# Kernel optimization log

Measured on AMD Instinct MI355X. Metric: run time of the kernel, lower is better.

## Reference

```python
import jax, jax.numpy as jnp
import numpy as np

B = 128
H = 512
S_TOK = 512
S_DESC = 128
N_NODES = 65536
MARGIN = 0.05
COS_EPS = 1e-8


def setup_inputs() -> dict:
    key = jax.random.key(0)
    ks = jax.random.split(key, 26)
    sc = 1.0 / np.sqrt(H)
    inp = {
        "token_feat": jax.random.normal(ks[0], (B, S_TOK, H), jnp.float32),
        "token_len": jnp.maximum(jax.random.randint(ks[1], (B,), 0, S_TOK), 1),
        "node_h": jax.random.normal(ks[2], (N_NODES, H), jnp.float32),
        "seg_ids": jnp.sort(jax.random.randint(ks[3], (N_NODES,), 0, B)),
        "desc_anchor_feat": jax.random.normal(ks[4], (B, S_DESC, H), jnp.float32),
        "desc_anchor_len": jnp.maximum(jax.random.randint(ks[5], (B,), 0, S_DESC), 1),
        "desc_neg_feat": jax.random.normal(ks[6], (B, S_DESC, H), jnp.float32),
        "desc_neg_len": jnp.maximum(jax.random.randint(ks[7], (B,), 0, S_DESC), 1),
        # attention params: Linear(H,H) weight/bias, Linear(H,1) weight/bias
        "Wt": jax.random.normal(ks[8], (H, H), jnp.float32) * sc,
        "bt": jax.random.normal(ks[9], (H,), jnp.float32) * sc,
        "vt": jax.random.normal(ks[10], (H,), jnp.float32) * sc,
        "ct": jax.random.normal(ks[11], (), jnp.float32) * sc,
        "Wa": jax.random.normal(ks[12], (H, H), jnp.float32) * sc,
        "ba": jax.random.normal(ks[13], (H,), jnp.float32) * sc,
        "va": jax.random.normal(ks[14], (H,), jnp.float32) * sc,
        "ca": jax.random.normal(ks[15], (), jnp.float32) * sc,
        "Wd": jax.random.normal(ks[16], (H, H), jnp.float32) * sc,
        "bd": jax.random.normal(ks[17], (H,), jnp.float32) * sc,
        "vd": jax.random.normal(ks[18], (H,), jnp.float32) * sc,
        "cd": jax.random.normal(ks[19], (), jnp.float32) * sc,
        "Wf": jax.random.normal(ks[20], (2 * H, H), jnp.float32) * sc,
        "bf": jax.random.normal(ks[21], (H,), jnp.float32) * sc,
    }
    return inp


def masked_attn_pool(feat, lens, W, b, v, c):
    # feat: [B,S,H]; lens: [B]. Masked softmax attention pooling == the
    # per-sample masked_select + softmax + bmm loop, vectorized.
    logits = jnp.einsum("bsh,h->bs", jnp.tanh(jnp.einsum("bsh,hk->bsk", feat, W) + b), v) + c
    mask = jnp.arange(feat.shape[1])[None, :] < lens[:, None]
    logits = jnp.where(mask, logits, -jnp.inf)
    w = jax.nn.softmax(logits, axis=1)  # [B,S]
    return jnp.einsum("bs,bsh->bh", w, feat)


def segment_attn_pool(h, seg, W, b, v, c, num_segments):
    # h: [N,H] packed node states; seg: [N] sample id. Per-segment softmax attn
    # pooling == the per-sample slice + softmax + bmm loop over tree_node_num.
    logits = jnp.tanh(h @ W + b) @ v + c  # [N]
    m = jax.ops.segment_max(logits, seg, num_segments=num_segments)
    e = jnp.exp(logits - m[seg])
    denom = jax.ops.segment_sum(e, seg, num_segments=num_segments)
    w = e / denom[seg]
    return jax.ops.segment_sum(w[:, None] * h, seg, num_segments=num_segments)


def cosine_sim(a, b):
    na = jnp.maximum(jnp.linalg.norm(a, axis=1), COS_EPS)
    nb = jnp.maximum(jnp.linalg.norm(b, axis=1), COS_EPS)
    return jnp.sum(a * b, axis=1) / (na * nb)


def reference(token_feat, token_len, node_h, seg_ids, desc_anchor_feat,
              desc_anchor_len, desc_neg_feat, desc_neg_len,
              Wt, bt, vt, ct, Wa, ba, va, ca, Wd, bd, vd, cd, Wf, bf):
    # token modality (use_token_attn, then use_tanh)
    tok = jnp.tanh(masked_attn_pool(token_feat, token_len, Wt, bt, vt, ct))
    # AST modality: use_tanh applies to node states BEFORE attention
    hn = jnp.tanh(node_h)
    ast = jnp.tanh(segment_attn_pool(hn, seg_ids, Wa, ba, va, ca, B))
    code_feat = jnp.tanh(jnp.concatenate([tok, ast], axis=1) @ Wf + bf)
    # desc modality: attn pool, use_tanh, then the extra unconditional tanh
    da = jnp.tanh(jnp.tanh(masked_attn_pool(desc_anchor_feat, desc_anchor_len, Wd, bd, vd, cd)))
    dn = jnp.tanh(jnp.tanh(masked_attn_pool(desc_neg_feat, desc_neg_len, Wd, bd, vd, cd)))
    anchor_sim = cosine_sim(code_feat, da)
    neg_sim = cosine_sim(code_feat, dn)
    loss = jnp.mean(jnp.maximum(MARGIN - anchor_sim + neg_sim, 1e-6))
    return loss
```

## Files before the change

kernel.cpp:

```cpp
#include <hip/hip_runtime.h>
#include <math.h>

#define HDIM 512
#define BATCH 128

typedef _Float16 f16x8 __attribute__((ext_vector_type(8)));
typedef float f32x4 __attribute__((ext_vector_type(4)));

__device__ __forceinline__ float fast_tanh(float x) {
  float e = __expf(2.0f * x);
  return 1.0f - 2.0f / (e + 1.0f);
}

__device__ __forceinline__ void gload_lds16(const void* g, void* l) {
  __builtin_amdgcn_global_load_lds(
      (const __attribute__((address_space(1))) unsigned int*)g,
      (__attribute__((address_space(3))) unsigned int*)l, 16, 0, 0);
}


__global__ __launch_bounds__(256) void cvt_frag_kernel(
    const float* __restrict__ tok, const float* __restrict__ node,
    const float* __restrict__ da, const float* __restrict__ dn,
    _Float16* __restrict__ A2tok, _Float16* __restrict__ A2node,
    _Float16* __restrict__ A2desc) {
  const int seg = blockIdx.y;
  const float* A;
  _Float16* A2;
  int M16, rb_base, rb_bits;
  bool do_tanh = false;
  if (seg == 0)      { A = tok;  A2 = A2tok;  M16 = 4096; rb_base = 0;    rb_bits = 12; }
  else if (seg == 1) { A = node; A2 = A2node; M16 = 4096; rb_base = 0;    rb_bits = 12; do_tanh = true; }
  else if (seg == 2) { A = da;   A2 = A2desc; M16 = 2048; rb_base = 0;    rb_bits = 10; }
  else               { A = dn;   A2 = A2desc; M16 = 2048; rb_base = 1024; rb_bits = 10; }
  const int lane = threadIdx.x & 63, wid = threadIdx.x >> 6;
  const int total = 16 << rb_bits;
  const int rl = lane & 15, kc = lane >> 4;
  for (int fl = blockIdx.x * 4 + wid; fl < total; fl += gridDim.x * 4) {
    const int frag = fl >> rb_bits;
    const int rb_local = fl & ((1 << rb_bits) - 1);
    const int rb = rb_base + rb_local;
    const int kt = frag >> 1, ks = frag & 1;
    const int row_src = rb_local * 16 + rl;
    const int k = kt * 64 + ks * 32 + kc * 8;
    const float4* src = (const float4*)(A + (size_t)row_src * HDIM + k);
    const float4 x = src[0];
    const float4 y = src[1];
    f16x8 h;
    if (do_tanh) {
      h[0] = (_Float16)fast_tanh(x.x); h[1] = (_Float16)fast_tanh(x.y);
      h[2] = (_Float16)fast_tanh(x.z); h[3] = (_Float16)fast_tanh(x.w);
      h[4] = (_Float16)fast_tanh(y.x); h[5] = (_Float16)fast_tanh(y.y);
      h[6] = (_Float16)fast_tanh(y.z); h[7] = (_Float16)fast_tanh(y.w);
    } else {
      h[0] = (_Float16)x.x; h[1] = (_Float16)x.y;
      h[2] = (_Float16)x.z; h[3] = (_Float16)x.w;
      h[4] = (_Float16)y.x; h[5] = (_Float16)y.y;
      h[6] = (_Float16)y.z; h[7] = (_Float16)y.w;
    }
    *(f16x8*)(A2 + ((size_t)frag * M16 + rb) * 512 + lane * 8) = h;
  }
}

__global__ __launch_bounds__(256) void cvt_w3_kernel(
    const float* __restrict__ Wt, const float* __restrict__ Wa,
    const float* __restrict__ Wd, _Float16* __restrict__ W2t,
    _Float16* __restrict__ W2a, _Float16* __restrict__ W2d) {
  const int i = blockIdx.x * 256 + threadIdx.x;
  if (i >= 512 * 64) return;
  const float* W = (blockIdx.y == 0) ? Wt : (blockIdx.y == 1) ? Wa : Wd;
  _Float16* W2 = (blockIdx.y == 0) ? W2t : (blockIdx.y == 1) ? W2a : W2d;
  const int n = i & 511, g = i >> 9;
  const int kt = g >> 3, cc = g & 7;
  f16x8 h;
#pragma unroll
  for (int j = 0; j < 8; ++j)
    h[j] = (_Float16)W[(size_t)(kt * 64 + cc * 8 + j) * HDIM + n];
  char* dst = (char*)W2 + ((size_t)kt * 512 + n) * 128 + ((cc * 16) ^ ((n & 7) << 4));
  *(f16x8*)dst = h;
}

__global__ __launch_bounds__(256, 2) void gemm_logits_frag_kernel(
    const _Float16* __restrict__ A2tok, const _Float16* __restrict__ A2node,
    const _Float16* __restrict__ A2desc,
    const _Float16* __restrict__ W2t, const _Float16* __restrict__ W2a,
    const _Float16* __restrict__ W2d,
    const float* __restrict__ bt, const float* __restrict__ vt,
    const float* __restrict__ ba, const float* __restrict__ va,
    const float* __restrict__ bd, const float* __restrict__ vd,
    float* __restrict__ logits_tok, float* __restrict__ logits_node,
    float* __restrict__ logits_desc) {
  __shared__ __align__(16) _Float16 Bs[2][256 * 64];

  const int tid = threadIdx.x;
  const int raw = (int)blockIdx.x;
  const int swz = (raw & 7) * 320 + (raw >> 3);

  int id, local;
  if (swz < 1024)      { id = 0; local = swz; }
  else if (swz < 2048) { id = 1; local = swz - 1024; }
  else                 { id = 2; local = swz - 2048; }
  const int mb = local >> 1, nb = local & 1;
  const _Float16* A2 = (id == 0) ? A2tok : (id == 1) ? A2node : A2desc;
  const _Float16* W2 = (id == 0) ? W2t : (id == 1) ? W2a : W2d;
  const float* bias = (id == 0) ? bt : (id == 1) ? ba : bd;
  const float* vvec = (id == 0) ? vt : (id == 1) ? va : vd;
  float* logits = (id == 0) ? logits_tok : (id == 1) ? logits_node : logits_desc;
  const int M16 = (id == 2) ? 2048 : 4096;
  const size_t m0 = (size_t)mb * 128;
  const int n0 = nb * 256;

  const int lane = tid & 63, wid = tid >> 6;
  const int tx = lane & 15, qd = lane >> 4;
  const int wm = wid >> 1;
  const int wn = wid & 1;

  const _Float16* aBase = A2 + ((size_t)(m0 >> 4) + wm * 4) * 512 + lane * 8;
  const char* gB = (const char*)W2 + (size_t)n0 * 128;

  f32x4 acc[4][8];
#pragma unroll
  for (int i = 0; i < 4; ++i)
#pragma unroll
    for (int j = 0; j < 8; ++j) acc[i][j] = (f32x4){0.f, 0.f, 0.f, 0.f};

  f16x8 aR[2][2][4];

  auto LOAD_A = [&](int par, int kt) {
#pragma unroll
    for (int ks = 0; ks < 2; ++ks)
#pragma unroll
      for (int i = 0; i < 4; ++i)
        aR[par][ks][i] =
            *(const f16x8*)(aBase + ((size_t)(kt * 2 + ks) * M16 + i) * 512);
  };
  auto STAGE_B = [&](int buf, int kt) {
    const char* b = gB + (size_t)kt * 65536;
#pragma unroll
    for (int p = 0; p < 8; ++p)
      gload_lds16(b + tid * 16 + p * 4096, (char*)Bs[buf] + tid * 16 + p * 4096);
  };
  auto COMPUTE = [&](int par, int buf) {
#pragma unroll
    for (int ks = 0; ks < 2; ++ks) {
#pragma unroll
      for (int half = 0; half < 2; ++half) {
        f16x8 bF[4];
#pragma unroll
        for (int f = 0; f < 4; ++f) {
          const int n = wn * 128 + (half * 4 + f) * 16 + tx;
          int by = n * 128 + ((ks * 64 + qd * 16) ^ ((n & 7) << 4));
          bF[f] = *(const f16x8*)((const char*)Bs[buf] + by);
        }
        __builtin_amdgcn_s_setprio(1);
#pragma unroll
        for (int i = 0; i < 4; ++i)
#pragma unroll
          for (int f = 0; f < 4; ++f)
            acc[i][half * 4 + f] = __builtin_amdgcn_mfma_f32_16x16x32_f16(
                aR[par][ks][i], bF[f], acc[i][half * 4 + f], 0, 0, 0);
        __builtin_amdgcn_s_setprio(0);
      }
    }
  };

  LOAD_A(0, 0);
  STAGE_B(0, 0);
#pragma unroll
  for (int t = 0; t < 8; ++t) {
    const int cur = t & 1;
    if (t < 7) {
      LOAD_A(cur ^ 1, t + 1);
      STAGE_B(cur ^ 1, t + 1);
      asm volatile("s_waitcnt vmcnt(16)" ::: "memory");
    } else {
      asm volatile("s_waitcnt vmcnt(0)" ::: "memory");
    }
    __builtin_amdgcn_s_barrier();
    asm volatile("" ::: "memory");
    COMPUTE(cur, cur);
    asm volatile("" ::: "memory");
    __builtin_amdgcn_s_barrier();
    asm volatile("" ::: "memory");
  }

  float vv[8], bb[8];
#pragma unroll
  for (int j = 0; j < 8; ++j) {
    const int n = n0 + wn * 128 + j * 16 + tx;
    vv[j] = vvec[n];
    bb[j] = bias[n];
  }
#pragma unroll
  for (int i = 0; i < 4; ++i) {
#pragma unroll
    for (int r = 0; r < 4; ++r) {
      float s = 0.0f;
#pragma unroll
      for (int j = 0; j < 8; ++j)
        s = fmaf(vv[j], fast_tanh(acc[i][j][r] + bb[j]), s);
      s += __shfl_xor(s, 1);
      s += __shfl_xor(s, 2);
      s += __shfl_xor(s, 4);
      s += __shfl_xor(s, 8);
      if (tx == 0)
        atomicAdd(&logits[m0 + wm * 64 + i * 16 + qd * 4 + r], s);
    }
  }
}


__global__ void zero_kernel(float* __restrict__ p, int n) {
  const int i = blockIdx.x * 256 + threadIdx.x;
  if (i < n) p[i] = 0.0f;
}

__global__ void seg_bounds_kernel(const int* __restrict__ seg, int N,
                                  int* __restrict__ seg_start) {
  const int b = threadIdx.x;
  if (b > BATCH) return;
  int lo = 0, hi = N;
  while (lo < hi) {
    const int mid = (lo + hi) >> 1;
    if (seg[mid] < b) lo = mid + 1; else hi = mid;
  }
  seg_start[b] = lo;
}

__global__ __launch_bounds__(256) void softmax_all_kernel(
    float* __restrict__ ltok, float* __restrict__ ldesc,
    float* __restrict__ lnode, const int* __restrict__ tlen,
    const int* __restrict__ dalen, const int* __restrict__ dnlen,
    const int* __restrict__ seg_start) {
  __shared__ float smax[4], ssum[4];
  const int b = blockIdx.x, mode = blockIdx.y, tid = threadIdx.x;
  float* l;
  int s0, s1, fill_end;
  if (mode == 0)      { l = ltok + (size_t)b * 512;          s0 = 0; s1 = tlen[b];  fill_end = 512; }
  else if (mode == 1) { l = ldesc + (size_t)b * 128;         s0 = 0; s1 = dalen[b]; fill_end = 128; }
  else if (mode == 2) { l = ldesc + 16384 + (size_t)b * 128; s0 = 0; s1 = dnlen[b]; fill_end = 128; }
  else                { l = lnode; s0 = seg_start[b]; s1 = seg_start[b + 1]; fill_end = -1; }

  float mymax = -1e30f;
  for (int s = s0 + tid; s < s1; s += 256) mymax = fmaxf(mymax, l[s]);
#pragma unroll
  for (int off = 32; off; off >>= 1) mymax = fmaxf(mymax, __shfl_xor(mymax, off));
  if ((tid & 63) == 0) smax[tid >> 6] = mymax;
  __syncthreads();
  const float bmax = fmaxf(fmaxf(smax[0], smax[1]), fmaxf(smax[2], smax[3]));
  float mysum = 0.0f;
  for (int s = s0 + tid; s < s1; s += 256) mysum += __expf(l[s] - bmax);
#pragma unroll
  for (int off = 32; off; off >>= 1) mysum += __shfl_xor(mysum, off);
  if ((tid & 63) == 0) ssum[tid >> 6] = mysum;
  __syncthreads();
  const float inv = 1.0f / (ssum[0] + ssum[1] + ssum[2] + ssum[3]);
  for (int s = s0 + tid; s < s1; s += 256) l[s] = __expf(l[s] - bmax) * inv;
  if (fill_end > 0)
    for (int s = s1 + tid; s < fill_end; s += 256) l[s] = 0.0f;
}

__device__ __forceinline__ unsigned frag_read2(
    const _Float16* __restrict__ A2, int M16, int row, int h) {
  const int frag = (h >> 6) * 2 + ((h >> 5) & 1);
  const int lane = (row & 15) + (((h >> 3) & 3) << 4);
  const size_t off = ((size_t)frag * M16 + (row >> 4)) * 512 + lane * 8 + (h & 7);
  return *(const unsigned*)((const char*)A2 + off * 2);
}

__global__ __launch_bounds__(256) void pool_masked_all_kernel(
    const _Float16* __restrict__ A2tok, const _Float16* __restrict__ A2desc,
    const float* __restrict__ ltok, const float* __restrict__ ldesc,
    float* __restrict__ tok_pool, float* __restrict__ da_pool,
    float* __restrict__ dn_pool) {
  const int b = blockIdx.x, c = blockIdx.y, tid = threadIdx.x;
  const _Float16* A2;
  const float* w;
  float* out;
  int M16, rbase, s0;
  if (c < 8)       { A2 = A2tok;  M16 = 4096; rbase = b * 512;         w = ltok;  out = tok_pool; s0 = c * 64; }
  else if (c < 10) { A2 = A2desc; M16 = 2048; rbase = b * 128;         w = ldesc; out = da_pool;  s0 = (c - 8) * 64; }
  else             { A2 = A2desc; M16 = 2048; rbase = 16384 + b * 128; w = ldesc; out = dn_pool;  s0 = (c - 10) * 64; }
  const int h = tid * 2;
  float ax = 0.0f, ay = 0.0f;
  for (int s = s0; s < s0 + 64; ++s) {
    const int row = rbase + s;
    const float wsc = w[row];
    if (wsc != 0.0f) {
      const unsigned u = frag_read2(A2, M16, row, h);
      const _Float16* hp = (const _Float16*)&u;
      ax = fmaf(wsc, (float)hp[0], ax);
      ay = fmaf(wsc, (float)hp[1], ay);
    }
  }
  atomicAdd(&out[b * HDIM + h], ax);
  atomicAdd(&out[b * HDIM + h + 1], ay);
}

__global__ __launch_bounds__(256) void pool_tiled_seg_kernel(
    const _Float16* __restrict__ A2, const float* __restrict__ w,
    const int* __restrict__ seg_start, float* __restrict__ pool) {
  const int b = blockIdx.x, c = blockIdx.y, tid = threadIdx.x;
  const int h = tid * 2;
  const int s0 = seg_start[b], s1 = seg_start[b + 1];
  const int nseg = s1 - s0;
  const int chunk = (nseg + (int)gridDim.y - 1) / (int)gridDim.y;
  const int a0 = s0 + c * chunk;
  const int a1 = min(s1, a0 + chunk);
  float ax = 0.0f, ay = 0.0f;
  for (int s = a0; s < a1; ++s) {
    const float wsc = w[s];
    const unsigned u = frag_read2(A2, 4096, s, h);
    const _Float16* hp = (const _Float16*)&u;
    ax = fmaf(wsc, (float)hp[0], ax);
    ay = fmaf(wsc, (float)hp[1], ay);
  }
  atomicAdd(&pool[b * HDIM + h], ax);
  atomicAdd(&pool[b * HDIM + h + 1], ay);
}

__global__ __launch_bounds__(256) void code_gemm_kernel(
    const float* __restrict__ tok_pool, const float* __restrict__ ast_pool,
    const float* __restrict__ Wf, float* __restrict__ parts) {
  __shared__ float catS[128][65];
  __shared__ float4 wfS[64][32];
  const int nb = blockIdx.x, kb = blockIdx.y, tid = threadIdx.x;
  const int k0 = kb * 64;
  const float* src = (k0 < 512) ? (tok_pool + k0) : (ast_pool + (k0 - 512));
  for (int i = tid; i < 128 * 16; i += 256) {
    const int r = i >> 4, c4 = i & 15;
    const float4 v = *(const float4*)(src + (size_t)r * HDIM + c4 * 4);
    catS[r][c4 * 4 + 0] = fast_tanh(v.x);
    catS[r][c4 * 4 + 1] = fast_tanh(v.y);
    catS[r][c4 * 4 + 2] = fast_tanh(v.z);
    catS[r][c4 * 4 + 3] = fast_tanh(v.w);
  }
  for (int i = tid; i < 64 * 32; i += 256) {
    const int r = i >> 5, c = i & 31;
    wfS[r][c] = *(const float4*)(Wf + (size_t)(k0 + r) * HDIM + nb * 128 + c * 4);
  }
  __syncthreads();
  const int tb = tid >> 4, tn = tid & 15;
  const int b0 = tb * 8, n0l = tn * 8;
  float acc[8][8];
#pragma unroll
  for (int i = 0; i < 8; ++i)
#pragma unroll
    for (int j = 0; j < 8; ++j) acc[i][j] = 0.0f;
  for (int k = 0; k < 64; ++k) {
    float a[8];
#pragma unroll
    for (int i = 0; i < 8; ++i) a[i] = catS[b0 + i][k];
    const float4 w0 = wfS[k][tn * 2], w1 = wfS[k][tn * 2 + 1];
    const float wv[8] = {w0.x, w0.y, w0.z, w0.w, w1.x, w1.y, w1.z, w1.w};
#pragma unroll
    for (int i = 0; i < 8; ++i)
#pragma unroll
      for (int j = 0; j < 8; ++j) acc[i][j] = fmaf(a[i], wv[j], acc[i][j]);
  }
  float* dst = parts + ((size_t)kb * 128) * HDIM + nb * 128;
#pragma unroll
  for (int i = 0; i < 8; ++i) {
    const float4 o0 = {acc[i][0], acc[i][1], acc[i][2], acc[i][3]};
    const float4 o1 = {acc[i][4], acc[i][5], acc[i][6], acc[i][7]};
    *(float4*)(dst + (size_t)(b0 + i) * HDIM + n0l) = o0;
    *(float4*)(dst + (size_t)(b0 + i) * HDIM + n0l + 4) = o1;
  }
}

__global__ __launch_bounds__(256) void sims_kernel(
    const float* __restrict__ parts, const float* __restrict__ bfv,
    const float* __restrict__ da_pool, const float* __restrict__ dn_pool,
    float* __restrict__ terms) {
  __shared__ float sr[4][5];
  const int b = blockIdx.x, tid = threadIdx.x;
  float c2 = 0, a2 = 0, n2 = 0, ca = 0, cn = 0;
  for (int i = tid; i < HDIM; i += 256) {
    float pre = bfv[i];
#pragma unroll
    for (int kb = 0; kb < 16; ++kb)
      pre += parts[((size_t)kb * 128 + b) * HDIM + i];
    const float cf = fast_tanh(pre);
    const float av = fast_tanh(fast_tanh(da_pool[(size_t)b * HDIM + i]));
    const float nv = fast_tanh(fast_tanh(dn_pool[(size_t)b * HDIM + i]));
    c2 = fmaf(cf, cf, c2); a2 = fmaf(av, av, a2); n2 = fmaf(nv, nv, n2);
    ca = fmaf(cf, av, ca); cn = fmaf(cf, nv, cn);
  }
#pragma unroll
  for (int off = 32; off; off >>= 1) {
    c2 += __shfl_xor(c2, off); a2 += __shfl_xor(a2, off); n2 += __shfl_xor(n2, off);
    ca += __shfl_xor(ca, off); cn += __shfl_xor(cn, off);
  }
  const int wv = tid >> 6;
  if ((tid & 63) == 0) {
    sr[wv][0] = c2; sr[wv][1] = a2; sr[wv][2] = n2; sr[wv][3] = ca; sr[wv][4] = cn;
  }
  __syncthreads();
  if (tid == 0) {
    c2 = sr[0][0] + sr[1][0] + sr[2][0] + sr[3][0];
    a2 = sr[0][1] + sr[1][1] + sr[2][1] + sr[3][1];
    n2 = sr[0][2] + sr[1][2] + sr[2][2] + sr[3][2];
    ca = sr[0][3] + sr[1][3] + sr[2][3] + sr[3][3];
    cn = sr[0][4] + sr[1][4] + sr[2][4] + sr[3][4];
    const float nc = fmaxf(sqrtf(c2), 1e-8f);
    const float na = fmaxf(sqrtf(a2), 1e-8f);
    const float nn = fmaxf(sqrtf(n2), 1e-8f);
    terms[b] = fmaxf(0.05f - ca / (nc * na) + cn / (nc * nn), 1e-6f);
  }
}

__global__ void loss_kernel(const float* __restrict__ terms, float* __restrict__ out) {
  const int tid = threadIdx.x;
  float v = terms[tid];
#pragma unroll
  for (int off = 32; off; off >>= 1) v += __shfl_xor(v, off);
  __shared__ float sr[2];
  if ((tid & 63) == 0) sr[tid >> 6] = v;
  __syncthreads();
  if (tid == 0) out[0] = (sr[0] + sr[1]) * (1.0f / (float)BATCH);
}


extern "C" void kernel_launch(void* const* d_in, const int* in_sizes, int n_in,
                              void* d_out, int out_size, void* d_ws, size_t ws_size,
                              hipStream_t stream) {
  (void)in_sizes; (void)n_in; (void)out_size; (void)ws_size;
  const float* token_feat = (const float*)d_in[0];
  const int*   token_len  = (const int*)d_in[1];
  const float* node_h     = (const float*)d_in[2];
  const int*   seg_ids    = (const int*)d_in[3];
  const float* da_feat    = (const float*)d_in[4];
  const int*   da_len     = (const int*)d_in[5];
  const float* dn_feat    = (const float*)d_in[6];
  const int*   dn_len     = (const int*)d_in[7];
  const float* Wt = (const float*)d_in[8];
  const float* bt = (const float*)d_in[9];
  const float* vt = (const float*)d_in[10];
  const float* Wa = (const float*)d_in[12];
  const float* ba = (const float*)d_in[13];
  const float* va = (const float*)d_in[14];
  const float* Wd = (const float*)d_in[16];
  const float* bd = (const float*)d_in[17];
  const float* vd = (const float*)d_in[18];
  const float* Wf  = (const float*)d_in[20];
  const float* bfv = (const float*)d_in[21];

  const int MTOK = 65536;
  const int MDESC2 = 32768;
  const int NNODES = 65536;

  float* ws = (float*)d_ws;
  float* logits_tok  = ws;
  float* logits_node = logits_tok + MTOK;
  float* logits_desc = logits_node + NNODES;
  float* tok_pool    = logits_desc + MDESC2;
  float* ast_pool    = tok_pool + 128 * HDIM;
  float* da_pool     = ast_pool + 128 * HDIM;
  float* dn_pool     = da_pool + 128 * HDIM;
  float* terms       = dn_pool + 128 * HDIM;
  int*   seg_start   = (int*)(terms + 128);
  float* parts       = (float*)(seg_start + 256);
  _Float16* W2t = (_Float16*)(parts + 16 * 128 * HDIM);
  _Float16* W2a = W2t + HDIM * HDIM;
  _Float16* W2d = W2a + HDIM * HDIM;
  _Float16* A2tok  = W2d + HDIM * HDIM;
  _Float16* A2node = A2tok + (size_t)MTOK * 512;
  _Float16* A2desc = A2node + (size_t)NNODES * 512;

  const int ZTOT = MTOK + NNODES + MDESC2 + 4 * 128 * HDIM;
  zero_kernel<<<dim3((ZTOT + 255) / 256), 256, 0, stream>>>(ws, ZTOT);
  seg_bounds_kernel<<<1, 256, 0, stream>>>(seg_ids, NNODES, seg_start);

  cvt_w3_kernel<<<dim3(128, 3), 256, 0, stream>>>(Wt, Wa, Wd, W2t, W2a, W2d);
  cvt_frag_kernel<<<dim3(4096, 4), 256, 0, stream>>>(
      token_feat, node_h, da_feat, dn_feat, A2tok, A2node, A2desc);

  gemm_logits_frag_kernel<<<2560, 256, 0, stream>>>(
      A2tok, A2node, A2desc, W2t, W2a, W2d,
      bt, vt, ba, va, bd, vd, logits_tok, logits_node, logits_desc);

  softmax_all_kernel<<<dim3(BATCH, 4), 256, 0, stream>>>(
      logits_tok, logits_desc, logits_node, token_len, da_len, dn_len, seg_start);

  pool_masked_all_kernel<<<dim3(BATCH, 12), 256, 0, stream>>>(
      A2tok, A2desc, logits_tok, logits_desc, tok_pool, da_pool, dn_pool);
  pool_tiled_seg_kernel<<<dim3(BATCH, 4), 256, 0, stream>>>(
      A2node, logits_node, seg_start, ast_pool);

  code_gemm_kernel<<<dim3(4, 16), 256, 0, stream>>>(tok_pool, ast_pool, Wf, parts);
  sims_kernel<<<BATCH, 256, 0, stream>>>(parts, bfv, da_pool, dn_pool, terms);
  loss_kernel<<<1, 128, 0, stream>>>(terms, (float*)d_out);
}
```

Baseline: 309.6 us.

## Fuse fp32-to-fp16 conversion into token/desc GEMM and pool from fp32 inputs

The token and description inputs are no longer converted into a separate fp16 fragment buffer. A new GEMM kernel loads fp32 A rows directly, converts them in registers and feeds the MFMAs, with staggered waitcnt pipelining across the two k-substeps. The masked pooling kernel now reads the original fp32 features instead of the fp16 fragments. Only the node path keeps the tanh+convert prepass. This removes a large write and re-read of intermediate fp16 data, but the GEMM reads twice as many A bytes and uses less efficient A access patterns.

```diff
diff --git a/kernel.cpp b/kernel.cpp
--- a/kernel.cpp
+++ b/kernel.cpp
@@ -19,46 +19,25 @@
 }
 
 
-__global__ __launch_bounds__(256) void cvt_frag_kernel(
-    const float* __restrict__ tok, const float* __restrict__ node,
-    const float* __restrict__ da, const float* __restrict__ dn,
-    _Float16* __restrict__ A2tok, _Float16* __restrict__ A2node,
-    _Float16* __restrict__ A2desc) {
-  const int seg = blockIdx.y;
-  const float* A;
-  _Float16* A2;
-  int M16, rb_base, rb_bits;
-  bool do_tanh = false;
-  if (seg == 0)      { A = tok;  A2 = A2tok;  M16 = 4096; rb_base = 0;    rb_bits = 12; }
-  else if (seg == 1) { A = node; A2 = A2node; M16 = 4096; rb_base = 0;    rb_bits = 12; do_tanh = true; }
-  else if (seg == 2) { A = da;   A2 = A2desc; M16 = 2048; rb_base = 0;    rb_bits = 10; }
-  else               { A = dn;   A2 = A2desc; M16 = 2048; rb_base = 1024; rb_bits = 10; }
+__global__ __launch_bounds__(256) void cvt_frag_node_kernel(
+    const float* __restrict__ node, _Float16* __restrict__ A2node) {
   const int lane = threadIdx.x & 63, wid = threadIdx.x >> 6;
-  const int total = 16 << rb_bits;
   const int rl = lane & 15, kc = lane >> 4;
-  for (int fl = blockIdx.x * 4 + wid; fl < total; fl += gridDim.x * 4) {
-    const int frag = fl >> rb_bits;
-    const int rb_local = fl & ((1 << rb_bits) - 1);
-    const int rb = rb_base + rb_local;
+  for (int fl = blockIdx.x * 4 + wid; fl < 65536; fl += gridDim.x * 4) {
+    const int frag = fl >> 12;
+    const int rb = fl & 4095;
     const int kt = frag >> 1, ks = frag & 1;
-    const int row_src = rb_local * 16 + rl;
+    const int row = rb * 16 + rl;
     const int k = kt * 64 + ks * 32 + kc * 8;
-    const float4* src = (const float4*)(A + (size_t)row_src * HDIM + k);
+    const float4* src = (const float4*)(node + (size_t)row * HDIM + k);
     const float4 x = src[0];
     const float4 y = src[1];
     f16x8 h;
-    if (do_tanh) {
-      h[0] = (_Float16)fast_tanh(x.x); h[1] = (_Float16)fast_tanh(x.y);
-      h[2] = (_Float16)fast_tanh(x.z); h[3] = (_Float16)fast_tanh(x.w);
-      h[4] = (_Float16)fast_tanh(y.x); h[5] = (_Float16)fast_tanh(y.y);
-      h[6] = (_Float16)fast_tanh(y.z); h[7] = (_Float16)fast_tanh(y.w);
-    } else {
-      h[0] = (_Float16)x.x; h[1] = (_Float16)x.y;
-      h[2] = (_Float16)x.z; h[3] = (_Float16)x.w;
-      h[4] = (_Float16)y.x; h[5] = (_Float16)y.y;
-      h[6] = (_Float16)y.z; h[7] = (_Float16)y.w;
-    }
-    *(f16x8*)(A2 + ((size_t)frag * M16 + rb) * 512 + lane * 8) = h;
+    h[0] = (_Float16)fast_tanh(x.x); h[1] = (_Float16)fast_tanh(x.y);
+    h[2] = (_Float16)fast_tanh(x.z); h[3] = (_Float16)fast_tanh(x.w);
+    h[4] = (_Float16)fast_tanh(y.x); h[5] = (_Float16)fast_tanh(y.y);
+    h[6] = (_Float16)fast_tanh(y.z); h[7] = (_Float16)fast_tanh(y.w);
+    *(f16x8*)(A2node + ((size_t)frag * 4096 + rb) * 512 + lane * 8) = h;
   }
 }
 
@@ -80,40 +59,22 @@
   *(f16x8*)dst = h;
 }
 
-__global__ __launch_bounds__(256, 2) void gemm_logits_frag_kernel(
-    const _Float16* __restrict__ A2tok, const _Float16* __restrict__ A2node,
-    const _Float16* __restrict__ A2desc,
-    const _Float16* __restrict__ W2t, const _Float16* __restrict__ W2a,
-    const _Float16* __restrict__ W2d,
-    const float* __restrict__ bt, const float* __restrict__ vt,
-    const float* __restrict__ ba, const float* __restrict__ va,
-    const float* __restrict__ bd, const float* __restrict__ vd,
-    float* __restrict__ logits_tok, float* __restrict__ logits_node,
-    float* __restrict__ logits_desc) {
+__global__ __launch_bounds__(256, 2) void gemm_logits_node_kernel(
+    const _Float16* __restrict__ A2, const _Float16* __restrict__ W2,
+    const float* __restrict__ bias, const float* __restrict__ vvec,
+    float* __restrict__ logits) {
   __shared__ __align__(16) _Float16 Bs[2][256 * 64];
 
   const int tid = threadIdx.x;
   const int raw = (int)blockIdx.x;
-  const int swz = (raw & 7) * 320 + (raw >> 3);
-
-  int id, local;
-  if (swz < 1024)      { id = 0; local = swz; }
-  else if (swz < 2048) { id = 1; local = swz - 1024; }
-  else                 { id = 2; local = swz - 2048; }
-  const int mb = local >> 1, nb = local & 1;
-  const _Float16* A2 = (id == 0) ? A2tok : (id == 1) ? A2node : A2desc;
-  const _Float16* W2 = (id == 0) ? W2t : (id == 1) ? W2a : W2d;
-  const float* bias = (id == 0) ? bt : (id == 1) ? ba : bd;
-  const float* vvec = (id == 0) ? vt : (id == 1) ? va : vd;
-  float* logits = (id == 0) ? logits_tok : (id == 1) ? logits_node : logits_desc;
-  const int M16 = (id == 2) ? 2048 : 4096;
+  const int swz = (raw & 7) * 128 + (raw >> 3);
+  const int mb = swz >> 1, nb = swz & 1;
   const size_t m0 = (size_t)mb * 128;
   const int n0 = nb * 256;
 
   const int lane = tid & 63, wid = tid >> 6;
   const int tx = lane & 15, qd = lane >> 4;
-  const int wm = wid >> 1;
-  const int wn = wid & 1;
+  const int wm = wid >> 1, wn = wid & 1;
 
   const _Float16* aBase = A2 + ((size_t)(m0 >> 4) + wm * 4) * 512 + lane * 8;
   const char* gB = (const char*)W2 + (size_t)n0 * 128;
@@ -132,7 +93,7 @@
 #pragma unroll
       for (int i = 0; i < 4; ++i)
         aR[par][ks][i] =
-            *(const f16x8*)(aBase + ((size_t)(kt * 2 + ks) * M16 + i) * 512);
+            *(const f16x8*)(aBase + ((size_t)(kt * 2 + ks) * 4096 + i) * 512);
   };
   auto STAGE_B = [&](int buf, int kt) {
     const char* b = gB + (size_t)kt * 65536;
@@ -179,6 +140,170 @@
     __builtin_amdgcn_s_barrier();
     asm volatile("" ::: "memory");
     COMPUTE(cur, cur);
+    asm volatile("" ::: "memory");
+    __builtin_amdgcn_s_barrier();
+    asm volatile("" ::: "memory");
+  }
+
+  float vv[8], bb[8];
+#pragma unroll
+  for (int j = 0; j < 8; ++j) {
+    const int n = n0 + wn * 128 + j * 16 + tx;
+    vv[j] = vvec[n];
+    bb[j] = bias[n];
+  }
+#pragma unroll
+  for (int i = 0; i < 4; ++i) {
+#pragma unroll
+    for (int r = 0; r < 4; ++r) {
+      float s = 0.0f;
+#pragma unroll
+      for (int j = 0; j < 8; ++j)
+        s = fmaf(vv[j], fast_tanh(acc[i][j][r] + bb[j]), s);
+      s += __shfl_xor(s, 1);
+      s += __shfl_xor(s, 2);
+      s += __shfl_xor(s, 4);
+      s += __shfl_xor(s, 8);
+      if (tx == 0)
+        atomicAdd(&logits[m0 + wm * 64 + i * 16 + qd * 4 + r], s);
+    }
+  }
+}
+
+__global__ __launch_bounds__(256, 2) void gemm_logits_f32a_kernel(
+    const float* __restrict__ A_tok, const float* __restrict__ A_da,
+    const float* __restrict__ A_dn,
+    const _Float16* __restrict__ W2t, const _Float16* __restrict__ W2d,
+    const float* __restrict__ bt, const float* __restrict__ vt,
+    const float* __restrict__ bd, const float* __restrict__ vd,
+    float* __restrict__ logits_tok, float* __restrict__ logits_desc) {
+  __shared__ __align__(16) _Float16 Bs[2][256 * 64];
+
+  const int tid = threadIdx.x;
+  const int raw = (int)blockIdx.x;
+  const int swz = (raw & 7) * 192 + (raw >> 3);
+
+  int id, local;
+  if (swz < 1024) { id = 0; local = swz; }
+  else            { id = 1; local = swz - 1024; }
+  const int mb = local >> 1, nb = local & 1;
+  const size_t m0 = (size_t)mb * 128;
+  const int n0 = nb * 256;
+  const float* A;
+  size_t m_src;
+  if (id == 0)            { A = A_tok; m_src = m0; }
+  else if (m0 < 16384)    { A = A_da;  m_src = m0; }
+  else                    { A = A_dn;  m_src = m0 - 16384; }
+  const _Float16* W2 = id ? W2d : W2t;
+  const float* bias = id ? bd : bt;
+  const float* vvec = id ? vd : vt;
+  float* logits = id ? logits_desc : logits_tok;
+
+  const int lane = tid & 63, wid = tid >> 6;
+  const int tx = lane & 15, qd = lane >> 4;
+  const int wm = wid >> 1, wn = wid & 1;
+
+  const float* aB32 = A + (m_src + wm * 64 + (lane & 15)) * (size_t)HDIM + (lane >> 4) * 8;
+  const char* gB = (const char*)W2 + (size_t)n0 * 128;
+
+  f32x4 acc[4][8];
+#pragma unroll
+  for (int i = 0; i < 4; ++i)
+#pragma unroll
+    for (int j = 0; j < 8; ++j) acc[i][j] = (f32x4){0.f, 0.f, 0.f, 0.f};
+
+  float4 f0[4][2], f1[4][2];
+  f16x8 aR[4];
+
+  auto STAGE_B = [&](int buf, int kt) {
+    const char* b = gB + (size_t)kt * 65536;
+#pragma unroll
+    for (int p = 0; p < 8; ++p)
+      gload_lds16(b + tid * 16 + p * 4096, (char*)Bs[buf] + tid * 16 + p * 4096);
+  };
+  auto LOADA0 = [&](int kt) {
+#pragma unroll
+    for (int i = 0; i < 4; ++i) {
+      const float* p = aB32 + (size_t)i * 8192 + kt * 64;
+      f0[i][0] = ((const float4*)p)[0];
+      f0[i][1] = ((const float4*)p)[1];
+    }
+  };
+  auto LOADA1 = [&](int kt) {
+#pragma unroll
+    for (int i = 0; i < 4; ++i) {
+      const float* p = aB32 + (size_t)i * 8192 + kt * 64 + 32;
+      f1[i][0] = ((const float4*)p)[0];
+      f1[i][1] = ((const float4*)p)[1];
+    }
+  };
+  auto CVT0 = [&]() {
+#pragma unroll
+    for (int i = 0; i < 4; ++i) {
+      f16x8 h;
+      h[0] = (_Float16)f0[i][0].x; h[1] = (_Float16)f0[i][0].y;
+      h[2] = (_Float16)f0[i][0].z; h[3] = (_Float16)f0[i][0].w;
+      h[4] = (_Float16)f0[i][1].x; h[5] = (_Float16)f0[i][1].y;
+      h[6] = (_Float16)f0[i][1].z; h[7] = (_Float16)f0[i][1].w;
+      aR[i] = h;
+    }
+  };
+  auto CVT1 = [&]() {
+#pragma unroll
+    for (int i = 0; i < 4; ++i) {
+      f16x8 h;
+      h[0] = (_Float16)f1[i][0].x; h[1] = (_Float16)f1[i][0].y;
+      h[2] = (_Float16)f1[i][0].z; h[3] = (_Float16)f1[i][0].w;
+      h[4] = (_Float16)f1[i][1].x; h[5] = (_Float16)f1[i][1].y;
+      h[6] = (_Float16)f1[i][1].z; h[7] = (_Float16)f1[i][1].w;
+      aR[i] = h;
+    }
+  };
+  auto MFMA_KS = [&](int buf, int ks) {
+#pragma unroll
+    for (int half = 0; half < 2; ++half) {
+      f16x8 bF[4];
+#pragma unroll
+      for (int f = 0; f < 4; ++f) {
+        const int n = wn * 128 + (half * 4 + f) * 16 + tx;
+        int by = n * 128 + ((ks * 64 + qd * 16) ^ ((n & 7) << 4));
+        bF[f] = *(const f16x8*)((const char*)Bs[buf] + by);
+      }
+      __builtin_amdgcn_s_setprio(1);
+#pragma unroll
+      for (int i = 0; i < 4; ++i)
+#pragma unroll
+        for (int f = 0; f < 4; ++f)
+          acc[i][half * 4 + f] = __builtin_amdgcn_mfma_f32_16x16x32_f16(
+              aR[i], bF[f], acc[i][half * 4 + f], 0, 0, 0);
+      __builtin_amdgcn_s_setprio(0);
+    }
+  };
+
+  STAGE_B(0, 0);
+  LOADA0(0);
+  LOADA1(0);
+#pragma unroll
+  for (int t = 0; t < 8; ++t) {
+    const int cur = t & 1;
+    if (t < 7) {
+      STAGE_B(cur ^ 1, t + 1);
+      asm volatile("s_waitcnt vmcnt(24)" ::: "memory");
+    } else {
+      asm volatile("s_waitcnt vmcnt(16)" ::: "memory");
+    }
+    __builtin_amdgcn_s_barrier();
+    asm volatile("" ::: "memory");
+    if (t < 7) asm volatile("s_waitcnt vmcnt(16)" ::: "memory");
+    else       asm volatile("s_waitcnt vmcnt(8)"  ::: "memory");
+    CVT0();
+    if (t < 7) LOADA0(t + 1);
+    MFMA_KS(cur, 0);
+    if (t < 7) asm volatile("s_waitcnt vmcnt(16)" ::: "memory");
+    else       asm volatile("s_waitcnt vmcnt(0)"  ::: "memory");
+    CVT1();
+    if (t < 7) LOADA1(t + 1);
+    MFMA_KS(cur, 1);
     asm volatile("" ::: "memory");
     __builtin_amdgcn_s_barrier();
     asm volatile("" ::: "memory");
@@ -260,41 +385,40 @@
     for (int s = s1 + tid; s < fill_end; s += 256) l[s] = 0.0f;
 }
 
+__global__ __launch_bounds__(256) void pool_masked_all_kernel(
+    const float* __restrict__ tok_feat, const float* __restrict__ da_feat,
+    const float* __restrict__ dn_feat, const float* __restrict__ ltok,
+    const float* __restrict__ ldesc, float* __restrict__ tok_pool,
+    float* __restrict__ da_pool, float* __restrict__ dn_pool) {
+  const int b = blockIdx.x, c = blockIdx.y, tid = threadIdx.x;
+  const float* feat;
+  const float* w;
+  float* out;
+  int S, s0;
+  if (c < 8)       { feat = tok_feat; S = 512; w = ltok + (size_t)b * 512;          out = tok_pool; s0 = c * 64; }
+  else if (c < 10) { feat = da_feat;  S = 128; w = ldesc + (size_t)b * 128;         out = da_pool;  s0 = (c - 8) * 64; }
+  else             { feat = dn_feat;  S = 128; w = ldesc + 16384 + (size_t)b * 128; out = dn_pool;  s0 = (c - 10) * 64; }
+  const int h = tid * 2;
+  const float* fb = feat + (size_t)b * S * HDIM + h;
+  float ax = 0.0f, ay = 0.0f;
+  for (int s = s0; s < s0 + 64; ++s) {
+    const float wsc = w[s];
+    if (wsc != 0.0f) {
+      const float2 f = *(const float2*)(fb + (size_t)s * HDIM);
+      ax = fmaf(wsc, f.x, ax);
+      ay = fmaf(wsc, f.y, ay);
+    }
+  }
+  atomicAdd(&out[b * HDIM + h], ax);
+  atomicAdd(&out[b * HDIM + h + 1], ay);
+}
+
 __device__ __forceinline__ unsigned frag_read2(
-    const _Float16* __restrict__ A2, int M16, int row, int h) {
+    const _Float16* __restrict__ A2, int row, int h) {
   const int frag = (h >> 6) * 2 + ((h >> 5) & 1);
   const int lane = (row & 15) + (((h >> 3) & 3) << 4);
-  const size_t off = ((size_t)frag * M16 + (row >> 4)) * 512 + lane * 8 + (h & 7);
+  const size_t off = ((size_t)frag * 4096 + (row >> 4)) * 512 + lane * 8 + (h & 7);
   return *(const unsigned*)((const char*)A2 + off * 2);
-}
-
-__global__ __launch_bounds__(256) void pool_masked_all_kernel(
-    const _Float16* __restrict__ A2tok, const _Float16* __restrict__ A2desc,
-    const float* __restrict__ ltok, const float* __restrict__ ldesc,
-    float* __restrict__ tok_pool, float* __restrict__ da_pool,
-    float* __restrict__ dn_pool) {
-  const int b = blockIdx.x, c = blockIdx.y, tid = threadIdx.x;
-  const _Float16* A2;
-  const float* w;
-  float* out;
-  int M16, rbase, s0;
-  if (c < 8)       { A2 = A2tok;  M16 = 4096; rbase = b * 512;         w = ltok;  out = tok_pool; s0 = c * 64; }
-  else if (c < 10) { A2 = A2desc; M16 = 2048; rbase = b * 128;         w = ldesc; out = da_pool;  s0 = (c - 8) * 64; }
-  else             { A2 = A2desc; M16 = 2048; rbase = 16384 + b * 128; w = ldesc; out = dn_pool;  s0 = (c - 10) * 64; }
-  const int h = tid * 2;
-  float ax = 0.0f, ay = 0.0f;
-  for (int s = s0; s < s0 + 64; ++s) {
-    const int row = rbase + s;
-    const float wsc = w[row];
-    if (wsc != 0.0f) {
-      const unsigned u = frag_read2(A2, M16, row, h);
-      const _Float16* hp = (const _Float16*)&u;
-      ax = fmaf(wsc, (float)hp[0], ax);
-      ay = fmaf(wsc, (float)hp[1], ay);
-    }
-  }
-  atomicAdd(&out[b * HDIM + h], ax);
-  atomicAdd(&out[b * HDIM + h + 1], ay);
 }
 
 __global__ __launch_bounds__(256) void pool_tiled_seg_kernel(
@@ -310,7 +434,7 @@
   float ax = 0.0f, ay = 0.0f;
   for (int s = a0; s < a1; ++s) {
     const float wsc = w[s];
-    const unsigned u = frag_read2(A2, 4096, s, h);
+    const unsigned u = frag_read2(A2, s, h);
     const _Float16* hp = (const _Float16*)&u;
     ax = fmaf(wsc, (float)hp[0], ax);
     ay = fmaf(wsc, (float)hp[1], ay);
@@ -463,27 +587,27 @@
   _Float16* W2t = (_Float16*)(parts + 16 * 128 * HDIM);
   _Float16* W2a = W2t + HDIM * HDIM;
   _Float16* W2d = W2a + HDIM * HDIM;
-  _Float16* A2tok  = W2d + HDIM * HDIM;
-  _Float16* A2node = A2tok + (size_t)MTOK * 512;
-  _Float16* A2desc = A2node + (size_t)NNODES * 512;
+  _Float16* A2node = W2d + HDIM * HDIM;
 
   const int ZTOT = MTOK + NNODES + MDESC2 + 4 * 128 * HDIM;
   zero_kernel<<<dim3((ZTOT + 255) / 256), 256, 0, stream>>>(ws, ZTOT);
   seg_bounds_kernel<<<1, 256, 0, stream>>>(seg_ids, NNODES, seg_start);
 
   cvt_w3_kernel<<<dim3(128, 3), 256, 0, stream>>>(Wt, Wa, Wd, W2t, W2a, W2d);
-  cvt_frag_kernel<<<dim3(4096, 4), 256, 0, stream>>>(
-      token_feat, node_h, da_feat, dn_feat, A2tok, A2node, A2desc);
-
-  gemm_logits_frag_kernel<<<2560, 256, 0, stream>>>(
-      A2tok, A2node, A2desc, W2t, W2a, W2d,
-      bt, vt, ba, va, bd, vd, logits_tok, logits_node, logits_desc);
+  cvt_frag_node_kernel<<<2048, 256, 0, stream>>>(node_h, A2node);
+
+  gemm_logits_f32a_kernel<<<1536, 256, 0, stream>>>(
+      token_feat, da_feat, dn_feat, W2t, W2d,
+      bt, vt, bd, vd, logits_tok, logits_desc);
+  gemm_logits_node_kernel<<<1024, 256, 0, stream>>>(
+      A2node, W2a, ba, va, logits_node);
 
   softmax_all_kernel<<<dim3(BATCH, 4), 256, 0, stream>>>(
       logits_tok, logits_desc, logits_node, token_len, da_len, dn_len, seg_start);
 
   pool_masked_all_kernel<<<dim3(BATCH, 12), 256, 0, stream>>>(
-      A2tok, A2desc, logits_tok, logits_desc, tok_pool, da_pool, dn_pool);
+      token_feat, da_feat, dn_feat, logits_tok, logits_desc,
+      tok_pool, da_pool, dn_pool);
   pool_tiled_seg_kernel<<<dim3(BATCH, 4), 256, 0, stream>>>(
       A2node, logits_node, seg_start, ast_pool);
 
```

Result: slower. 347.2 us (+12.2%).
